# Optimization experiments

Measured on AMD Instinct MI355X. Metric: run time of the kernel, lower is better.

Reference implementation:

```python
import jax, jax.numpy as jnp
import numpy as np

T, H, I, E, TOPK = 1024, 1024, 2048, 8, 2


def setup_inputs() -> dict:
    key = jax.random.key(0)
    k1, k2, k3, k4, k5, k6 = jax.random.split(key, 6)
    hidden_states = jax.random.normal(k1, (T, H), dtype=jnp.float32)
    expert_affinities = jax.random.uniform(k2, (T, E), dtype=jnp.float32)
    expert_index = jax.random.randint(k3, (T, TOPK), 0, E, dtype=jnp.int64)
    # Expert GLU MLP weights: gate/up [E,H,I], down [E,I,H]
    w_gate = jax.random.normal(k4, (E, H, I), dtype=jnp.float32) / np.sqrt(H)
    w_up = jax.random.normal(k5, (E, H, I), dtype=jnp.float32) / np.sqrt(H)
    w_down = jax.random.normal(k6, (E, I, H), dtype=jnp.float32) / np.sqrt(I)
    return {
        "hidden_states": hidden_states,
        "expert_affinities": expert_affinities,
        "expert_index": expert_index,
        "w_gate": w_gate,
        "w_up": w_up,
        "w_down": w_down,
        "seq_len": T,
    }


def reference(hidden_states, expert_affinities, expert_index, w_gate, w_up, w_down, seq_len):
    # Gather top-k affinities and renormalize (normalize_top_k_affinities=True)
    topk_aff = jnp.take_along_axis(expert_affinities, expert_index, axis=1)  # [T,K]
    topk_aff = topk_aff / jnp.sum(topk_aff, axis=1, keepdims=True)
    # Dense combine weights [T,E] (scatter of normalized top-k affinities)
    t_idx = jnp.arange(hidden_states.shape[0])[:, None]
    combine = jnp.zeros((hidden_states.shape[0], w_gate.shape[0]),
                        dtype=hidden_states.dtype).at[t_idx, expert_index].add(topk_aff)
    # GLU expert MLP for all experts (E small, grouped-GEMM form)
    g = jnp.einsum("th,ehi->tei", hidden_states, w_gate)  # [T,E,I]
    u = jnp.einsum("th,ehi->tei", hidden_states, w_up)    # [T,E,I]
    act = jax.nn.silu(g) * u                               # [T,E,I]
    # Down-projection fused with affinity-weighted combine
    out = jnp.einsum("tei,eih,te->th", act, w_down, combine)  # [T,H]
    return out
```

## Files before the change

### kernel.cpp

```cpp
#include <hip/hip_runtime.h>
#include <hip/hip_bf16.h>
#include <math.h>

#define T_ 1024
#define H_ 1024
#define I_ 2048
#define E_ 8
#define NSLOT 2048

#define BM 128
#define BK 32
#define BN1 64
#define BN2 64
#define NCHUNK_CAP 24
#define SPLITK2 2

typedef __attribute__((ext_vector_type(8))) short bf16x8;
typedef __attribute__((ext_vector_type(4))) float f32x4;
typedef __attribute__((ext_vector_type(4))) unsigned uint4v;
typedef __attribute__((ext_vector_type(2))) unsigned uint2v;

#define MFMA_BF16 __builtin_amdgcn_mfma_f32_16x16x32_bf16

__device__ __forceinline__ short f2bf(float f) {
  union { float f; unsigned u; } v; v.f = f;
  unsigned r = v.u + 0x7FFFu + ((v.u >> 16) & 1u);
  return (short)(r >> 16);
}
__device__ __forceinline__ unsigned cvtpk(float lo, float hi) {
  unsigned r;
  asm("v_cvt_pk_bf16_f32 %0, %1, %2" : "=v"(r) : "v"(lo), "v"(hi));
  return r;
}
__device__ __forceinline__ void gll16(const void* g, void* l) {
  __builtin_amdgcn_global_load_lds(
      (const __attribute__((address_space(1))) void*)g,
      (__attribute__((address_space(3))) void*)l, 16, 0, 0);
}

__device__ __forceinline__ void pipe_barrier6() {
  __builtin_amdgcn_sched_barrier(0);
  asm volatile("s_waitcnt vmcnt(6) lgkmcnt(0)" ::: "memory");
  __builtin_amdgcn_s_barrier();
  __builtin_amdgcn_sched_barrier(0);
}
__device__ __forceinline__ void drain_barrier() {
  __builtin_amdgcn_sched_barrier(0);
  asm volatile("s_waitcnt vmcnt(0) lgkmcnt(0)" ::: "memory");
  __builtin_amdgcn_s_barrier();
  __builtin_amdgcn_sched_barrier(0);
}

__device__ __forceinline__ unsigned bswz(int n, int kbyte) {
  return (unsigned)(n * 64 + (kbyte ^ (((n >> 2) & 3) << 4)));
}
__device__ __forceinline__ int rswz(int row) { return (row >> 1) & 3; }
__device__ __forceinline__ unsigned tile_addr(int row, int g) {
  return (unsigned)(row * 64 + (((g ^ rswz(row)) & 3) << 4));
}

__global__ __launch_bounds__(256) void k_prep_build(
    const float* __restrict__ hs, short* __restrict__ hs_bf,
    const float* __restrict__ aff, const int* __restrict__ eidx,
    int* __restrict__ meta, int* __restrict__ slot_tok, float* __restrict__ slot_w) {
  int i = (blockIdx.x * 256 + threadIdx.x) * 8;
  float4 v0 = *(const float4*)&hs[i];
  float4 v1 = *(const float4*)&hs[i + 4];
  uint4v p;
  p.x = cvtpk(v0.x, v0.y); p.y = cvtpk(v0.z, v0.w);
  p.z = cvtpk(v1.x, v1.y); p.w = cvtpk(v1.z, v1.w);
  *(uint4v*)&hs_bf[i] = p;

  if (blockIdx.x != 0) return;
  __shared__ int cnt[E_];
  __shared__ int soff[E_ + 1];
  int t = threadIdx.x;
  if (t < E_) cnt[t] = 0;
  __syncthreads();
  int e0a[4], e1a[4], r0a[4], r1a[4];
  float w0a[4], w1a[4];
#pragma unroll
  for (int j = 0; j < 4; ++j) {
    int tok = t + 256 * j;
    int e0 = eidx[tok * 2 + 0];
    int e1 = eidx[tok * 2 + 1];
    float a0 = aff[tok * E_ + e0];
    float a1 = aff[tok * E_ + e1];
    float inv = 1.0f / (a0 + a1);
    r0a[j] = atomicAdd(&cnt[e0], 1);
    r1a[j] = atomicAdd(&cnt[e1], 1);
    e0a[j] = e0; e1a[j] = e1;
    w0a[j] = a0 * inv; w1a[j] = a1 * inv;
  }
  __syncthreads();
  if (t == 0) {
    int s = 0;
    for (int e = 0; e < E_; ++e) { soff[e] = s; s += cnt[e]; }
    soff[E_] = s;
    int nc = 0;
    for (int e = 0; e < E_; ++e)
      for (int c = soff[e]; c < soff[e] + cnt[e]; c += BM)
        meta[16 + nc++] = e | (c << 8);
    meta[9] = nc;
  }
  __syncthreads();
  if (t <= E_) meta[t] = soff[t];
#pragma unroll
  for (int j = 0; j < 4; ++j) {
    int tok = t + 256 * j;
    int s0 = soff[e0a[j]] + r0a[j];
    int s1 = soff[e1a[j]] + r1a[j];
    slot_tok[s0] = tok; slot_w[s0] = w0a[j];
    slot_tok[s1] = tok; slot_w[s1] = w1a[j];
  }
}

__global__ __launch_bounds__(256, 3) void k_gemm1(
    const short* __restrict__ hs_bf, const float* __restrict__ wg,
    const float* __restrict__ wu, const int* __restrict__ meta,
    const int* __restrict__ slot_tok, short* __restrict__ act) {
  int nch = meta[9];
  if (blockIdx.y >= nch) return;
  int ck = meta[16 + blockIdx.y];
  int e = ck & 255;
  int row0 = ck >> 8;
  int rows = min(BM, meta[1 + e] - row0);
  int i0 = blockIdx.x * BN1;

  __shared__ short sA[4][BM * BK];
  __shared__ short sB[2][2][BN1 * BK];

  int tid = threadIdx.x;
  int lane = tid & 63;
  int w = tid >> 6;
  int wm = w >> 1, wn = w & 1;
  int lr = lane & 15;
  int g = lane >> 4;

  const float* wgE = wg + (size_t)e * H_ * I_;
  const float* wuE = wu + (size_t)e * H_ * I_;

  int r_a0 = 32 * w + (lane >> 2);
  int r_a1 = r_a0 + 16;
  int tok0 = slot_tok[row0 + min(r_a0, rows - 1)];
  int tok1 = slot_tok[row0 + min(r_a1, rows - 1)];
  const short* srcA0 = hs_bf + (size_t)tok0 * H_ + ((((lane & 3) ^ rswz(r_a0)) & 3) << 3);
  const short* srcA1 = hs_bf + (size_t)tok1 * H_ + ((((lane & 3) ^ rswz(r_a1)) & 3) << 3);

  int mat = tid >> 7;
  int kq = (tid >> 4) & 7;
  int nq = tid & 15;
  const float* srcB = (mat ? wuE : wgE) + (size_t)(4 * kq) * I_ + i0 + 4 * nq;

  f32x4 accg[4][2], accu[4][2];
#pragma unroll
  for (int mf = 0; mf < 4; ++mf)
#pragma unroll
    for (int nf = 0; nf < 2; ++nf) {
      accg[mf][nf] = (f32x4){0.f, 0.f, 0.f, 0.f};
      accu[mf][nf] = (f32x4){0.f, 0.f, 0.f, 0.f};
    }

  f32x4 bs0[4], bs1[4];

  const int NT = H_ / BK;

  gll16(srcA0, &sA[0][(32 * w) * 32]);
  gll16(srcA1, &sA[0][(32 * w + 16) * 32]);
#pragma unroll
  for (int j = 0; j < 4; ++j) bs0[j] = *(const f32x4*)(srcB + (size_t)j * I_);
  gll16(srcA0 + BK, &sA[1][(32 * w) * 32]);
  gll16(srcA1 + BK, &sA[1][(32 * w + 16) * 32]);
#pragma unroll
  for (int j = 0; j < 4; ++j) bs1[j] = *(const f32x4*)(srcB + (size_t)(BK + j) * I_);
  {
    char* dst = (char*)&sB[0][mat][0];
#pragma unroll
    for (int c = 0; c < 4; ++c) {
      int n = 4 * nq + c;
      uint2v wv;
      wv.x = cvtpk(bs0[0][c], bs0[1][c]);
      wv.y = cvtpk(bs0[2][c], bs0[3][c]);
      *(uint2v*)(dst + tile_addr(n, kq >> 1) + ((kq & 1) << 3)) = wv;
    }
  }
  drain_barrier();

#define G1_ITER(U, bsL, bsC) do {                                              \
    int t_ = base + (U);                                                       \
    const char* curA = (const char*)&sA[t_ & 3][0];                            \
    if (t_ + 2 < NT) {                                                         \
      short* nxtA = &sA[(t_ + 2) & 3][0];                                      \
      gll16(srcA0 + (size_t)(t_ + 2) * BK, nxtA + (32 * w) * 32);              \
      gll16(srcA1 + (size_t)(t_ + 2) * BK, nxtA + (32 * w + 16) * 32);         \
      const float* sb = srcB + (size_t)(t_ + 2) * BK * I_;                     \
      bsL[0] = *(const f32x4*)(sb);                                            \
      bsL[1] = *(const f32x4*)(sb + I_);                                       \
      bsL[2] = *(const f32x4*)(sb + 2 * I_);                                   \
      bsL[3] = *(const f32x4*)(sb + 3 * I_);                                   \
    }                                                                          \
    bf16x8 a0 = *(const bf16x8*)(curA + tile_addr(wm * 64 + lr, g));           \
    bf16x8 a1 = *(const bf16x8*)(curA + tile_addr(wm * 64 + 16 + lr, g));      \
    bf16x8 a2 = *(const bf16x8*)(curA + tile_addr(wm * 64 + 32 + lr, g));      \
    bf16x8 a3 = *(const bf16x8*)(curA + tile_addr(wm * 64 + 48 + lr, g));      \
    const char* pg = (const char*)&sB[(U)][0][0];                              \
    const char* pu = (const char*)&sB[(U)][1][0];                              \
    unsigned ob0 = tile_addr(wn * 32 + lr, g);                                 \
    unsigned ob1 = tile_addr(wn * 32 + 16 + lr, g);                            \
    bf16x8 g0 = *(const bf16x8*)(pg + ob0);                                    \
    bf16x8 g1 = *(const bf16x8*)(pg + ob1);                                    \
    bf16x8 u0 = *(const bf16x8*)(pu + ob0);                                    \
    bf16x8 u1 = *(const bf16x8*)(pu + ob1);                                    \
    accg[0][0] = MFMA_BF16(a0, g0, accg[0][0], 0, 0, 0);                       \
    accg[0][1] = MFMA_BF16(a0, g1, accg[0][1], 0, 0, 0);                       \
    accg[1][0] = MFMA_BF16(a1, g0, accg[1][0], 0, 0, 0);                       \
    accg[1][1] = MFMA_BF16(a1, g1, accg[1][1], 0, 0, 0);                       \
    accg[2][0] = MFMA_BF16(a2, g0, accg[2][0], 0, 0, 0);                       \
    accg[2][1] = MFMA_BF16(a2, g1, accg[2][1], 0, 0, 0);                       \
    accg[3][0] = MFMA_BF16(a3, g0, accg[3][0], 0, 0, 0);                       \
    accg[3][1] = MFMA_BF16(a3, g1, accg[3][1], 0, 0, 0);                       \
    accu[0][0] = MFMA_BF16(a0, u0, accu[0][0], 0, 0, 0);                       \
    accu[0][1] = MFMA_BF16(a0, u1, accu[0][1], 0, 0, 0);                       \
    accu[1][0] = MFMA_BF16(a1, u0, accu[1][0], 0, 0, 0);                       \
    accu[1][1] = MFMA_BF16(a1, u1, accu[1][1], 0, 0, 0);                       \
    accu[2][0] = MFMA_BF16(a2, u0, accu[2][0], 0, 0, 0);                       \
    accu[2][1] = MFMA_BF16(a2, u1, accu[2][1], 0, 0, 0);                       \
    accu[3][0] = MFMA_BF16(a3, u0, accu[3][0], 0, 0, 0);                       \
    accu[3][1] = MFMA_BF16(a3, u1, accu[3][1], 0, 0, 0);                       \
    if (t_ + 1 < NT) {                                                         \
      char* dst = (char*)&sB[(U) ^ 1][mat][0];                                 \
      _Pragma("unroll")                                                        \
      for (int c = 0; c < 4; ++c) {                                            \
        int n = 4 * nq + c;                                                    \
        uint2v wv;                                                             \
        wv.x = cvtpk(bsC[0][c], bsC[1][c]);                                    \
        wv.y = cvtpk(bsC[2][c], bsC[3][c]);                                    \
        *(uint2v*)(dst + tile_addr(n, kq >> 1) + ((kq & 1) << 3)) = wv;        \
      }                                                                        \
    }                                                                          \
    pipe_barrier6();                                                           \
  } while (0)

  for (int base = 0; base < NT; base += 2) {
    G1_ITER(0, bs0, bs1);
    G1_ITER(1, bs1, bs0);
  }
#undef G1_ITER

#pragma unroll
  for (int mf = 0; mf < 4; ++mf) {
#pragma unroll
    for (int r = 0; r < 4; ++r) {
      int m = wm * 64 + mf * 16 + g * 4 + r;
      if (m < rows) {
#pragma unroll
        for (int nf = 0; nf < 2; ++nf) {
          float gv = accg[mf][nf][r];
          float uv = accu[mf][nf][r];
          float sg = 1.0f / (1.0f + __expf(-gv));
          act[(size_t)(row0 + m) * I_ + i0 + wn * 32 + nf * 16 + lr] = f2bf(gv * sg * uv);
        }
      }
    }
  }
}

__global__ __launch_bounds__(512, 4) void k_gemm2(
    const short* __restrict__ act, const float* __restrict__ wd,
    const int* __restrict__ meta, const int* __restrict__ slot_tok,
    const float* __restrict__ slot_w, float* __restrict__ out) {
  int nch = meta[9];
  if (blockIdx.y >= nch) return;
  int ck = meta[16 + blockIdx.y];
  int e = ck & 255;
  int row0 = ck >> 8;
  int rows = min(BM, meta[1 + e] - row0);
  int h0 = blockIdx.x * BN2;
  int kbase = blockIdx.z * (I_ / SPLITK2);

  __shared__ short sA[4][BM * BK];
  __shared__ short sB[2][BN2 * BK];

  int tid = threadIdx.x;
  int lane = tid & 63;
  int w = tid >> 6;
  int wm = w >> 1, wn = w & 1;
  int lr = lane & 15;
  int lk = (lane >> 4) * 8;

  const float* wdE = wd + (size_t)e * I_ * H_;

  int ra = min(16 * w + (lane >> 2), rows - 1);
  const short* srcA = act + (size_t)(row0 + ra) * I_ + kbase + (lane & 3) * 8;
  int up = tid >> 5;
  int n2 = (tid & 31) * 2;
  const float* srcB = wdE + (size_t)(kbase + 2 * up) * H_ + h0 + n2;

  f32x4 acc[2][2];
#pragma unroll
  for (int mr = 0; mr < 2; ++mr)
#pragma unroll
    for (int nr = 0; nr < 2; ++nr)
      acc[mr][nr] = (f32x4){0.f, 0.f, 0.f, 0.f};

  float2 bs[4][2];

#pragma unroll
  for (int p = 0; p < 3; ++p) {
    gll16(srcA + p * BK, &sA[p][w * 512]);
    bs[p][0] = *(const float2*)(srcB + (size_t)(p * BK) * H_);
    bs[p][1] = *(const float2*)(srcB + (size_t)(p * BK + 1) * H_);
  }
  *(unsigned*)((char*)&sB[0][0] + bswz(n2, 4 * up))     = cvtpk(bs[0][0].x, bs[0][1].x);
  *(unsigned*)((char*)&sB[0][0] + bswz(n2 + 1, 4 * up)) = cvtpk(bs[0][0].y, bs[0][1].y);
  drain_barrier();

  const int NT = (I_ / SPLITK2) / BK;

#define G2_ITER(U, base_) do {                                                 \
    int t_ = (base_) + (U);                                                    \
    if (t_ + 3 < NT) {                                                         \
      int k3 = (t_ + 3) * BK;                                                  \
      gll16(srcA + k3, &sA[((U) + 3) & 3][w * 512]);                           \
      bs[((U) + 3) & 3][0] = *(const float2*)(srcB + (size_t)k3 * H_);         \
      bs[((U) + 3) & 3][1] = *(const float2*)(srcB + (size_t)(k3 + 1) * H_);   \
    }                                                                          \
    bf16x8 a0 = *(const bf16x8*)&sA[(U)][(wm * 32 + lr) * BK + lk];            \
    bf16x8 a1 = *(const bf16x8*)&sA[(U)][(wm * 32 + 16 + lr) * BK + lk];       \
    bf16x8 b0 = *(const bf16x8*)((const char*)&sB[(U) & 1][0]                  \
                                 + bswz(wn * 32 + lr, lk * 2));                \
    bf16x8 b1 = *(const bf16x8*)((const char*)&sB[(U) & 1][0]                  \
                                 + bswz(wn * 32 + 16 + lr, lk * 2));           \
    acc[0][0] = MFMA_BF16(a0, b0, acc[0][0], 0, 0, 0);                         \
    acc[0][1] = MFMA_BF16(a0, b1, acc[0][1], 0, 0, 0);                         \
    acc[1][0] = MFMA_BF16(a1, b0, acc[1][0], 0, 0, 0);                         \
    acc[1][1] = MFMA_BF16(a1, b1, acc[1][1], 0, 0, 0);                         \
    if (t_ + 1 < NT) {                                                         \
      int s_ = ((U) + 1) & 3;                                                  \
      *(unsigned*)((char*)&sB[((U) + 1) & 1][0] + bswz(n2, 4 * up))            \
          = cvtpk(bs[s_][0].x, bs[s_][1].x);                                   \
      *(unsigned*)((char*)&sB[((U) + 1) & 1][0] + bswz(n2 + 1, 4 * up))        \
          = cvtpk(bs[s_][0].y, bs[s_][1].y);                                   \
    }                                                                          \
    pipe_barrier6();                                                           \
  } while (0)

  for (int base = 0; base < NT; base += 4) {
    G2_ITER(0, base);
    G2_ITER(1, base);
    G2_ITER(2, base);
    G2_ITER(3, base);
  }
#undef G2_ITER

#pragma unroll
  for (int mr = 0; mr < 2; ++mr) {
#pragma unroll
    for (int r = 0; r < 4; ++r) {
      int m = wm * 32 + mr * 16 + (lane >> 4) * 4 + r;
      if (m < rows) {
        int gs = row0 + m;
        float wc = slot_w[gs];
        int tok = slot_tok[gs];
#pragma unroll
        for (int nr = 0; nr < 2; ++nr)
          atomicAdd(&out[(size_t)tok * H_ + h0 + wn * 32 + nr * 16 + lr],
                    acc[mr][nr][r] * wc);
      }
    }
  }
}

extern "C" void kernel_launch(void* const* d_in, const int* in_sizes, int n_in,
                              void* d_out, int out_size, void* d_ws, size_t ws_size,
                              hipStream_t stream) {
  const float* hs   = (const float*)d_in[0];
  const float* aff  = (const float*)d_in[1];
  const int*   eidx = (const int*)d_in[2];
  const float* wg   = (const float*)d_in[3];
  const float* wu   = (const float*)d_in[4];
  const float* wd   = (const float*)d_in[5];
  float* out = (float*)d_out;

  char* ws = (char*)d_ws;
  int*   meta     = (int*)ws;
  int*   slot_tok = (int*)(ws + 256);
  float* slot_w   = (float*)(ws + 256 + NSLOT * 4);
  short* hs_bf    = (short*)(ws + 256 + NSLOT * 8);
  short* act      = (short*)(ws + 256 + NSLOT * 8 + (size_t)T_ * H_ * 2);

  hipMemsetAsync(d_out, 0, (size_t)out_size * sizeof(float), stream);
  k_prep_build<<<(T_ * H_) / (256 * 8), 256, 0, stream>>>(
      hs, hs_bf, aff, eidx, meta, slot_tok, slot_w);
  k_gemm1<<<dim3(I_ / BN1, NCHUNK_CAP), 256, 0, stream>>>(
      hs_bf, wg, wu, meta, slot_tok, act);
  k_gemm2<<<dim3(H_ / BN2, NCHUNK_CAP, SPLITK2), 512, 0, stream>>>(
      act, wd, meta, slot_tok, slot_w, out);
}
```

Measured before the change: 101.5 us.

## Process two K-tiles per barrier with deeper B prefetch in both expert GEMMs

Both grouped GEMM kernels now handle two K-tiles per barrier phase, using a four-stage LDS ring for A and B. Global loads of the fp32 weights are issued four tiles ahead in two register sets. This halves the number of workgroup barriers and deepens the latency hiding for the weight stream. In exchange it uses more LDS and registers, and k_gemm1's occupancy hint drops from 3 to 2 blocks per CU, which may reduce latency tolerance.

```diff
diff --git a/kernel.cpp b/kernel.cpp
--- a/kernel.cpp
+++ b/kernel.cpp
@@ -38,9 +38,15 @@
       (__attribute__((address_space(3))) void*)l, 16, 0, 0);
 }
 
-__device__ __forceinline__ void pipe_barrier6() {
-  __builtin_amdgcn_sched_barrier(0);
-  asm volatile("s_waitcnt vmcnt(6) lgkmcnt(0)" ::: "memory");
+__device__ __forceinline__ void pipe_barrier8() {
+  __builtin_amdgcn_sched_barrier(0);
+  asm volatile("s_waitcnt vmcnt(8) lgkmcnt(0)" ::: "memory");
+  __builtin_amdgcn_s_barrier();
+  __builtin_amdgcn_sched_barrier(0);
+}
+__device__ __forceinline__ void pipe_barrier4() {
+  __builtin_amdgcn_sched_barrier(0);
+  asm volatile("s_waitcnt vmcnt(4) lgkmcnt(0)" ::: "memory");
   __builtin_amdgcn_s_barrier();
   __builtin_amdgcn_sched_barrier(0);
 }
@@ -50,6 +56,7 @@
   __builtin_amdgcn_s_barrier();
   __builtin_amdgcn_sched_barrier(0);
 }
+__device__ __forceinline__ void no_barrier() {}
 
 __device__ __forceinline__ unsigned bswz(int n, int kbyte) {
   return (unsigned)(n * 64 + (kbyte ^ (((n >> 2) & 3) << 4)));
@@ -115,7 +122,7 @@
   }
 }
 
-__global__ __launch_bounds__(256, 3) void k_gemm1(
+__global__ __launch_bounds__(256, 2) void k_gemm1(
     const short* __restrict__ hs_bf, const float* __restrict__ wg,
     const float* __restrict__ wu, const int* __restrict__ meta,
     const int* __restrict__ slot_tok, short* __restrict__ act) {
@@ -128,7 +135,7 @@
   int i0 = blockIdx.x * BN1;
 
   __shared__ short sA[4][BM * BK];
-  __shared__ short sB[2][2][BN1 * BK];
+  __shared__ short sB[4][2][BN1 * BK];
 
   int tid = threadIdx.x;
   int lane = tid & 63;
@@ -161,50 +168,40 @@
       accu[mf][nf] = (f32x4){0.f, 0.f, 0.f, 0.f};
     }
 
-  f32x4 bs0[4], bs1[4];
+  f32x4 xA0[4], xA1[4], xB0[4], xB1[4];
 
   const int NT = H_ / BK;
 
-  gll16(srcA0, &sA[0][(32 * w) * 32]);
-  gll16(srcA1, &sA[0][(32 * w + 16) * 32]);
-#pragma unroll
-  for (int j = 0; j < 4; ++j) bs0[j] = *(const f32x4*)(srcB + (size_t)j * I_);
-  gll16(srcA0 + BK, &sA[1][(32 * w) * 32]);
-  gll16(srcA1 + BK, &sA[1][(32 * w + 16) * 32]);
-#pragma unroll
-  for (int j = 0; j < 4; ++j) bs1[j] = *(const f32x4*)(srcB + (size_t)(BK + j) * I_);
-  {
-    char* dst = (char*)&sB[0][mat][0];
-#pragma unroll
-    for (int c = 0; c < 4; ++c) {
-      int n = 4 * nq + c;
-      uint2v wv;
-      wv.x = cvtpk(bs0[0][c], bs0[1][c]);
-      wv.y = cvtpk(bs0[2][c], bs0[3][c]);
-      *(uint2v*)(dst + tile_addr(n, kq >> 1) + ((kq & 1) << 3)) = wv;
-    }
-  }
-  drain_barrier();
-
-#define G1_ITER(U, bsL, bsC) do {                                              \
-    int t_ = base + (U);                                                       \
-    const char* curA = (const char*)&sA[t_ & 3][0];                            \
-    if (t_ + 2 < NT) {                                                         \
-      short* nxtA = &sA[(t_ + 2) & 3][0];                                      \
-      gll16(srcA0 + (size_t)(t_ + 2) * BK, nxtA + (32 * w) * 32);              \
-      gll16(srcA1 + (size_t)(t_ + 2) * BK, nxtA + (32 * w + 16) * 32);         \
-      const float* sb = srcB + (size_t)(t_ + 2) * BK * I_;                     \
-      bsL[0] = *(const f32x4*)(sb);                                            \
-      bsL[1] = *(const f32x4*)(sb + I_);                                       \
-      bsL[2] = *(const f32x4*)(sb + 2 * I_);                                   \
-      bsL[3] = *(const f32x4*)(sb + 3 * I_);                                   \
+#define G1_GLL(T) do {                                                         \
+    gll16(srcA0 + (size_t)(T) * BK, &sA[(T) & 3][(32 * w) * 32]);              \
+    gll16(srcA1 + (size_t)(T) * BK, &sA[(T) & 3][(32 * w + 16) * 32]);         \
+  } while (0)
+#define G1_LOADB(C, T) do {                                                    \
+    const float* sb_ = srcB + (size_t)(T) * BK * I_;                           \
+    C[0] = *(const f32x4*)(sb_);                                               \
+    C[1] = *(const f32x4*)(sb_ + I_);                                          \
+    C[2] = *(const f32x4*)(sb_ + 2 * I_);                                      \
+    C[3] = *(const f32x4*)(sb_ + 3 * I_);                                      \
+  } while (0)
+#define G1_CONV(T, C) do {                                                     \
+    char* dst_ = (char*)&sB[(T) & 3][mat][0];                                  \
+    _Pragma("unroll")                                                          \
+    for (int c_ = 0; c_ < 4; ++c_) {                                           \
+      int n_ = 4 * nq + c_;                                                    \
+      uint2v wv_;                                                              \
+      wv_.x = cvtpk(C[0][c_], C[1][c_]);                                       \
+      wv_.y = cvtpk(C[2][c_], C[3][c_]);                                       \
+      *(uint2v*)(dst_ + tile_addr(n_, kq >> 1) + ((kq & 1) << 3)) = wv_;       \
     }                                                                          \
+  } while (0)
+#define G1_COMPUTE(T) do {                                                     \
+    const char* curA = (const char*)&sA[(T) & 3][0];                           \
+    const char* pg = (const char*)&sB[(T) & 3][0][0];                          \
+    const char* pu = (const char*)&sB[(T) & 3][1][0];                          \
     bf16x8 a0 = *(const bf16x8*)(curA + tile_addr(wm * 64 + lr, g));           \
     bf16x8 a1 = *(const bf16x8*)(curA + tile_addr(wm * 64 + 16 + lr, g));      \
     bf16x8 a2 = *(const bf16x8*)(curA + tile_addr(wm * 64 + 32 + lr, g));      \
     bf16x8 a3 = *(const bf16x8*)(curA + tile_addr(wm * 64 + 48 + lr, g));      \
-    const char* pg = (const char*)&sB[(U)][0][0];                              \
-    const char* pu = (const char*)&sB[(U)][1][0];                              \
     unsigned ob0 = tile_addr(wn * 32 + lr, g);                                 \
     unsigned ob1 = tile_addr(wn * 32 + 16 + lr, g);                            \
     bf16x8 g0 = *(const bf16x8*)(pg + ob0);                                    \
@@ -227,25 +224,35 @@
     accu[2][1] = MFMA_BF16(a2, u1, accu[2][1], 0, 0, 0);                       \
     accu[3][0] = MFMA_BF16(a3, u0, accu[3][0], 0, 0, 0);                       \
     accu[3][1] = MFMA_BF16(a3, u1, accu[3][1], 0, 0, 0);                       \
-    if (t_ + 1 < NT) {                                                         \
-      char* dst = (char*)&sB[(U) ^ 1][mat][0];                                 \
-      _Pragma("unroll")                                                        \
-      for (int c = 0; c < 4; ++c) {                                            \
-        int n = 4 * nq + c;                                                    \
-        uint2v wv;                                                             \
-        wv.x = cvtpk(bsC[0][c], bsC[1][c]);                                    \
-        wv.y = cvtpk(bsC[2][c], bsC[3][c]);                                    \
-        *(uint2v*)(dst + tile_addr(n, kq >> 1) + ((kq & 1) << 3)) = wv;        \
-      }                                                                        \
-    }                                                                          \
-    pipe_barrier6();                                                           \
-  } while (0)
-
-  for (int base = 0; base < NT; base += 2) {
-    G1_ITER(0, bs0, bs1);
-    G1_ITER(1, bs1, bs0);
-  }
-#undef G1_ITER
+  } while (0)
+#define G1_PHASE(T0, LA, LB, CA, CB, BAR) do {                                 \
+    if ((T0) + 2 < NT) { G1_GLL((T0) + 2); G1_GLL((T0) + 3); }                 \
+    __builtin_amdgcn_sched_barrier(0);                                         \
+    if ((T0) + 4 < NT) { G1_LOADB(LA, (T0) + 4); G1_LOADB(LB, (T0) + 5); }     \
+    G1_COMPUTE(T0);                                                            \
+    G1_COMPUTE((T0) + 1);                                                      \
+    if ((T0) + 2 < NT) { G1_CONV((T0) + 2, CA); G1_CONV((T0) + 3, CB); }       \
+    BAR();                                                                     \
+  } while (0)
+
+  G1_GLL(0); G1_GLL(1); G1_GLL(2); G1_GLL(3);
+  G1_LOADB(xB0, 0); G1_LOADB(xB1, 1);
+  G1_CONV(0, xB0); G1_CONV(1, xB1);
+  G1_LOADB(xA0, 2); G1_LOADB(xA1, 3);
+  drain_barrier();
+
+  for (int T0 = 0; T0 < 28; T0 += 4) {
+    G1_PHASE(T0,     xB0, xB1, xA0, xA1, pipe_barrier8);
+    G1_PHASE(T0 + 2, xA0, xA1, xB0, xB1, pipe_barrier8);
+  }
+  G1_PHASE(28, xB0, xB1, xA0, xA1, drain_barrier);
+  G1_PHASE(30, xA0, xA1, xB0, xB1, no_barrier);
+
+#undef G1_PHASE
+#undef G1_COMPUTE
+#undef G1_CONV
+#undef G1_LOADB
+#undef G1_GLL
 
 #pragma unroll
   for (int mf = 0; mf < 4; ++mf) {
@@ -279,7 +286,7 @@
   int kbase = blockIdx.z * (I_ / SPLITK2);
 
   __shared__ short sA[4][BM * BK];
-  __shared__ short sB[2][BN2 * BK];
+  __shared__ short sB[4][BN2 * BK];
 
   int tid = threadIdx.x;
   int lane = tid & 63;
@@ -303,55 +310,60 @@
     for (int nr = 0; nr < 2; ++nr)
       acc[mr][nr] = (f32x4){0.f, 0.f, 0.f, 0.f};
 
-  float2 bs[4][2];
-
-#pragma unroll
-  for (int p = 0; p < 3; ++p) {
-    gll16(srcA + p * BK, &sA[p][w * 512]);
-    bs[p][0] = *(const float2*)(srcB + (size_t)(p * BK) * H_);
-    bs[p][1] = *(const float2*)(srcB + (size_t)(p * BK + 1) * H_);
-  }
-  *(unsigned*)((char*)&sB[0][0] + bswz(n2, 4 * up))     = cvtpk(bs[0][0].x, bs[0][1].x);
-  *(unsigned*)((char*)&sB[0][0] + bswz(n2 + 1, 4 * up)) = cvtpk(bs[0][0].y, bs[0][1].y);
-  drain_barrier();
+  float2 yA0[2], yA1[2], yB0[2], yB1[2];
 
   const int NT = (I_ / SPLITK2) / BK;
 
-#define G2_ITER(U, base_) do {                                                 \
-    int t_ = (base_) + (U);                                                    \
-    if (t_ + 3 < NT) {                                                         \
-      int k3 = (t_ + 3) * BK;                                                  \
-      gll16(srcA + k3, &sA[((U) + 3) & 3][w * 512]);                           \
-      bs[((U) + 3) & 3][0] = *(const float2*)(srcB + (size_t)k3 * H_);         \
-      bs[((U) + 3) & 3][1] = *(const float2*)(srcB + (size_t)(k3 + 1) * H_);   \
-    }                                                                          \
-    bf16x8 a0 = *(const bf16x8*)&sA[(U)][(wm * 32 + lr) * BK + lk];            \
-    bf16x8 a1 = *(const bf16x8*)&sA[(U)][(wm * 32 + 16 + lr) * BK + lk];       \
-    bf16x8 b0 = *(const bf16x8*)((const char*)&sB[(U) & 1][0]                  \
+#define G2_GLL(T) gll16(srcA + (size_t)(T) * BK, &sA[(T) & 3][w * 512])
+#define G2_LOADB(C, T) do {                                                    \
+    C[0] = *(const float2*)(srcB + (size_t)((T) * BK) * H_);                   \
+    C[1] = *(const float2*)(srcB + (size_t)((T) * BK + 1) * H_);               \
+  } while (0)
+#define G2_CONV(T, C) do {                                                     \
+    char* dst_ = (char*)&sB[(T) & 3][0];                                       \
+    *(unsigned*)(dst_ + bswz(n2, 4 * up))     = cvtpk(C[0].x, C[1].x);         \
+    *(unsigned*)(dst_ + bswz(n2 + 1, 4 * up)) = cvtpk(C[0].y, C[1].y);         \
+  } while (0)
+#define G2_COMPUTE(T) do {                                                     \
+    bf16x8 a0 = *(const bf16x8*)&sA[(T) & 3][(wm * 32 + lr) * BK + lk];        \
+    bf16x8 a1 = *(const bf16x8*)&sA[(T) & 3][(wm * 32 + 16 + lr) * BK + lk];   \
+    bf16x8 b0 = *(const bf16x8*)((const char*)&sB[(T) & 3][0]                  \
                                  + bswz(wn * 32 + lr, lk * 2));                \
-    bf16x8 b1 = *(const bf16x8*)((const char*)&sB[(U) & 1][0]                  \
+    bf16x8 b1 = *(const bf16x8*)((const char*)&sB[(T) & 3][0]                  \
                                  + bswz(wn * 32 + 16 + lr, lk * 2));           \
     acc[0][0] = MFMA_BF16(a0, b0, acc[0][0], 0, 0, 0);                         \
     acc[0][1] = MFMA_BF16(a0, b1, acc[0][1], 0, 0, 0);                         \
     acc[1][0] = MFMA_BF16(a1, b0, acc[1][0], 0, 0, 0);                         \
     acc[1][1] = MFMA_BF16(a1, b1, acc[1][1], 0, 0, 0);                         \
-    if (t_ + 1 < NT) {                                                         \
-      int s_ = ((U) + 1) & 3;                                                  \
-      *(unsigned*)((char*)&sB[((U) + 1) & 1][0] + bswz(n2, 4 * up))            \
-          = cvtpk(bs[s_][0].x, bs[s_][1].x);                                   \
-      *(unsigned*)((char*)&sB[((U) + 1) & 1][0] + bswz(n2 + 1, 4 * up))        \
-          = cvtpk(bs[s_][0].y, bs[s_][1].y);                                   \
-    }                                                                          \
-    pipe_barrier6();                                                           \
-  } while (0)
-
-  for (int base = 0; base < NT; base += 4) {
-    G2_ITER(0, base);
-    G2_ITER(1, base);
-    G2_ITER(2, base);
-    G2_ITER(3, base);
-  }
-#undef G2_ITER
+  } while (0)
+#define G2_PHASE(T0, LA, LB, CA, CB, BAR) do {                                 \
+    if ((T0) + 2 < NT) { G2_GLL((T0) + 2); G2_GLL((T0) + 3); }                 \
+    __builtin_amdgcn_sched_barrier(0);                                         \
+    if ((T0) + 4 < NT) { G2_LOADB(LA, (T0) + 4); G2_LOADB(LB, (T0) + 5); }     \
+    G2_COMPUTE(T0);                                                            \
+    G2_COMPUTE((T0) + 1);                                                      \
+    if ((T0) + 2 < NT) { G2_CONV((T0) + 2, CA); G2_CONV((T0) + 3, CB); }       \
+    BAR();                                                                     \
+  } while (0)
+
+  G2_GLL(0); G2_GLL(1); G2_GLL(2); G2_GLL(3);
+  G2_LOADB(yB0, 0); G2_LOADB(yB1, 1);
+  G2_CONV(0, yB0); G2_CONV(1, yB1);
+  G2_LOADB(yA0, 2); G2_LOADB(yA1, 3);
+  drain_barrier();
+
+  for (int T0 = 0; T0 < 28; T0 += 4) {
+    G2_PHASE(T0,     yB0, yB1, yA0, yA1, pipe_barrier4);
+    G2_PHASE(T0 + 2, yA0, yA1, yB0, yB1, pipe_barrier4);
+  }
+  G2_PHASE(28, yB0, yB1, yA0, yA1, drain_barrier);
+  G2_PHASE(30, yA0, yA1, yB0, yB1, no_barrier);
+
+#undef G2_PHASE
+#undef G2_COMPUTE
+#undef G2_CONV
+#undef G2_LOADB
+#undef G2_GLL
 
 #pragma unroll
   for (int mr = 0; mr < 2; ++mr) {
```

After: 105.9 us. 4.3% more time.

## Share gathered A tile across two N-tiles in 512-thread gemm1 blocks

Applied to the files above, without the earlier changes.

Doubles the k_gemm1 block to 512 threads, with two 256-thread groups each computing a different 64-column slice of the intermediate dimension. Both groups share one gathered hidden-state A tile in LDS, so each thread issues one gather load instead of two and the grid halves in x. The pipeline wait count drops to vmcnt(5) to match the smaller number of outstanding loads per thread. The cost is more LDS per block for the doubled B buffers and fewer, larger blocks, which can lower occupancy.

```diff
diff --git a/kernel.cpp b/kernel.cpp
--- a/kernel.cpp
+++ b/kernel.cpp
@@ -38,6 +38,12 @@
       (__attribute__((address_space(3))) void*)l, 16, 0, 0);
 }
 
+__device__ __forceinline__ void pipe_barrier5() {
+  __builtin_amdgcn_sched_barrier(0);
+  asm volatile("s_waitcnt vmcnt(5) lgkmcnt(0)" ::: "memory");
+  __builtin_amdgcn_s_barrier();
+  __builtin_amdgcn_sched_barrier(0);
+}
 __device__ __forceinline__ void pipe_barrier6() {
   __builtin_amdgcn_sched_barrier(0);
   asm volatile("s_waitcnt vmcnt(6) lgkmcnt(0)" ::: "memory");
@@ -115,7 +121,7 @@
   }
 }
 
-__global__ __launch_bounds__(256, 3) void k_gemm1(
+__global__ __launch_bounds__(512, 2) void k_gemm1(
     const short* __restrict__ hs_bf, const float* __restrict__ wg,
     const float* __restrict__ wu, const int* __restrict__ meta,
     const int* __restrict__ slot_tok, short* __restrict__ act) {
@@ -125,31 +131,32 @@
   int e = ck & 255;
   int row0 = ck >> 8;
   int rows = min(BM, meta[1 + e] - row0);
-  int i0 = blockIdx.x * BN1;
 
   __shared__ short sA[4][BM * BK];
-  __shared__ short sB[2][2][BN1 * BK];
+  __shared__ short sB[2][2][2][BN1 * BK];
 
   int tid = threadIdx.x;
   int lane = tid & 63;
-  int w = tid >> 6;
-  int wm = w >> 1, wn = w & 1;
+  int w8 = tid >> 6;
+  int grp = tid >> 8;
+  int wg_ = w8 & 3;
+  int wm = wg_ >> 1, wn = wg_ & 1;
   int lr = lane & 15;
   int g = lane >> 4;
 
+  int i0 = blockIdx.x * (2 * BN1) + grp * BN1;
+
   const float* wgE = wg + (size_t)e * H_ * I_;
   const float* wuE = wu + (size_t)e * H_ * I_;
 
-  int r_a0 = 32 * w + (lane >> 2);
-  int r_a1 = r_a0 + 16;
-  int tok0 = slot_tok[row0 + min(r_a0, rows - 1)];
-  int tok1 = slot_tok[row0 + min(r_a1, rows - 1)];
-  const short* srcA0 = hs_bf + (size_t)tok0 * H_ + ((((lane & 3) ^ rswz(r_a0)) & 3) << 3);
-  const short* srcA1 = hs_bf + (size_t)tok1 * H_ + ((((lane & 3) ^ rswz(r_a1)) & 3) << 3);
-
-  int mat = tid >> 7;
-  int kq = (tid >> 4) & 7;
-  int nq = tid & 15;
+  int r_a = 16 * w8 + (lane >> 2);
+  int tokA = slot_tok[row0 + min(r_a, rows - 1)];
+  const short* srcA = hs_bf + (size_t)tokA * H_ + ((((lane & 3) ^ rswz(r_a)) & 3) << 3);
+
+  int g_tid = tid & 255;
+  int mat = g_tid >> 7;
+  int kq = (g_tid >> 4) & 7;
+  int nq = g_tid & 15;
   const float* srcB = (mat ? wuE : wgE) + (size_t)(4 * kq) * I_ + i0 + 4 * nq;
 
   f32x4 accg[4][2], accu[4][2];
@@ -165,46 +172,33 @@
 
   const int NT = H_ / BK;
 
-  gll16(srcA0, &sA[0][(32 * w) * 32]);
-  gll16(srcA1, &sA[0][(32 * w + 16) * 32]);
-#pragma unroll
-  for (int j = 0; j < 4; ++j) bs0[j] = *(const f32x4*)(srcB + (size_t)j * I_);
-  gll16(srcA0 + BK, &sA[1][(32 * w) * 32]);
-  gll16(srcA1 + BK, &sA[1][(32 * w + 16) * 32]);
-#pragma unroll
-  for (int j = 0; j < 4; ++j) bs1[j] = *(const f32x4*)(srcB + (size_t)(BK + j) * I_);
-  {
-    char* dst = (char*)&sB[0][mat][0];
-#pragma unroll
-    for (int c = 0; c < 4; ++c) {
-      int n = 4 * nq + c;
-      uint2v wv;
-      wv.x = cvtpk(bs0[0][c], bs0[1][c]);
-      wv.y = cvtpk(bs0[2][c], bs0[3][c]);
-      *(uint2v*)(dst + tile_addr(n, kq >> 1) + ((kq & 1) << 3)) = wv;
-    }
-  }
-  drain_barrier();
-
-#define G1_ITER(U, bsL, bsC) do {                                              \
-    int t_ = base + (U);                                                       \
-    const char* curA = (const char*)&sA[t_ & 3][0];                            \
-    if (t_ + 2 < NT) {                                                         \
-      short* nxtA = &sA[(t_ + 2) & 3][0];                                      \
-      gll16(srcA0 + (size_t)(t_ + 2) * BK, nxtA + (32 * w) * 32);              \
-      gll16(srcA1 + (size_t)(t_ + 2) * BK, nxtA + (32 * w + 16) * 32);         \
-      const float* sb = srcB + (size_t)(t_ + 2) * BK * I_;                     \
-      bsL[0] = *(const f32x4*)(sb);                                            \
-      bsL[1] = *(const f32x4*)(sb + I_);                                       \
-      bsL[2] = *(const f32x4*)(sb + 2 * I_);                                   \
-      bsL[3] = *(const f32x4*)(sb + 3 * I_);                                   \
+#define G1_GLL(T) gll16(srcA + (size_t)(T) * BK, &sA[(T) & 3][(16 * w8) * 32])
+#define G1_LOADB(C, T) do {                                                    \
+    const float* sb_ = srcB + (size_t)(T) * BK * I_;                           \
+    C[0] = *(const f32x4*)(sb_);                                               \
+    C[1] = *(const f32x4*)(sb_ + I_);                                          \
+    C[2] = *(const f32x4*)(sb_ + 2 * I_);                                      \
+    C[3] = *(const f32x4*)(sb_ + 3 * I_);                                      \
+  } while (0)
+#define G1_CONV(BUF, C) do {                                                   \
+    char* dst_ = (char*)&sB[(BUF)][grp][mat][0];                               \
+    _Pragma("unroll")                                                          \
+    for (int c_ = 0; c_ < 4; ++c_) {                                           \
+      int n_ = 4 * nq + c_;                                                    \
+      uint2v wv_;                                                              \
+      wv_.x = cvtpk(C[0][c_], C[1][c_]);                                       \
+      wv_.y = cvtpk(C[2][c_], C[3][c_]);                                       \
+      *(uint2v*)(dst_ + tile_addr(n_, kq >> 1) + ((kq & 1) << 3)) = wv_;       \
     }                                                                          \
+  } while (0)
+#define G1_COMPUTE(T, BUF) do {                                                \
+    const char* curA = (const char*)&sA[(T) & 3][0];                           \
+    const char* pg = (const char*)&sB[(BUF)][grp][0][0];                       \
+    const char* pu = (const char*)&sB[(BUF)][grp][1][0];                       \
     bf16x8 a0 = *(const bf16x8*)(curA + tile_addr(wm * 64 + lr, g));           \
     bf16x8 a1 = *(const bf16x8*)(curA + tile_addr(wm * 64 + 16 + lr, g));      \
     bf16x8 a2 = *(const bf16x8*)(curA + tile_addr(wm * 64 + 32 + lr, g));      \
     bf16x8 a3 = *(const bf16x8*)(curA + tile_addr(wm * 64 + 48 + lr, g));      \
-    const char* pg = (const char*)&sB[(U)][0][0];                              \
-    const char* pu = (const char*)&sB[(U)][1][0];                              \
     unsigned ob0 = tile_addr(wn * 32 + lr, g);                                 \
     unsigned ob1 = tile_addr(wn * 32 + 16 + lr, g);                            \
     bf16x8 g0 = *(const bf16x8*)(pg + ob0);                                    \
@@ -227,25 +221,34 @@
     accu[2][1] = MFMA_BF16(a2, u1, accu[2][1], 0, 0, 0);                       \
     accu[3][0] = MFMA_BF16(a3, u0, accu[3][0], 0, 0, 0);                       \
     accu[3][1] = MFMA_BF16(a3, u1, accu[3][1], 0, 0, 0);                       \
-    if (t_ + 1 < NT) {                                                         \
-      char* dst = (char*)&sB[(U) ^ 1][mat][0];                                 \
-      _Pragma("unroll")                                                        \
-      for (int c = 0; c < 4; ++c) {                                            \
-        int n = 4 * nq + c;                                                    \
-        uint2v wv;                                                             \
-        wv.x = cvtpk(bsC[0][c], bsC[1][c]);                                    \
-        wv.y = cvtpk(bsC[2][c], bsC[3][c]);                                    \
-        *(uint2v*)(dst + tile_addr(n, kq >> 1) + ((kq & 1) << 3)) = wv;        \
-      }                                                                        \
+  } while (0)
+#define G1_ITER(U, bsL, bsC) do {                                              \
+    int t_ = base + (U);                                                       \
+    if (t_ + 2 < NT) {                                                         \
+      G1_GLL(t_ + 2);                                                          \
+      G1_LOADB(bsL, t_ + 2);                                                   \
     }                                                                          \
-    pipe_barrier6();                                                           \
+    G1_COMPUTE(t_, (U));                                                       \
+    if (t_ + 1 < NT) G1_CONV((U) ^ 1, bsC);                                    \
+    pipe_barrier5();                                                           \
   } while (0)
+
+  G1_GLL(0);
+  G1_GLL(1);
+  G1_LOADB(bs0, 0);
+  G1_LOADB(bs1, 1);
+  G1_CONV(0, bs0);
+  drain_barrier();
 
   for (int base = 0; base < NT; base += 2) {
     G1_ITER(0, bs0, bs1);
     G1_ITER(1, bs1, bs0);
   }
 #undef G1_ITER
+#undef G1_COMPUTE
+#undef G1_CONV
+#undef G1_LOADB
+#undef G1_GLL
 
 #pragma unroll
   for (int mf = 0; mf < 4; ++mf) {
@@ -392,7 +395,7 @@
   hipMemsetAsync(d_out, 0, (size_t)out_size * sizeof(float), stream);
   k_prep_build<<<(T_ * H_) / (256 * 8), 256, 0, stream>>>(
       hs, hs_bf, aff, eidx, meta, slot_tok, slot_w);
-  k_gemm1<<<dim3(I_ / BN1, NCHUNK_CAP), 256, 0, stream>>>(
+  k_gemm1<<<dim3(I_ / (2 * BN1), NCHUNK_CAP), 512, 0, stream>>>(
       hs_bf, wg, wu, meta, slot_tok, act);
   k_gemm2<<<dim3(H_ / BN2, NCHUNK_CAP, SPLITK2), 512, 0, stream>>>(
       act, wd, meta, slot_tok, slot_w, out);
```

After: 138.4 us. +36.3%, slower.
